# Kernel tuning notes

Measured on AMD Instinct MI355X. Metric: run time of the kernel, lower is better.

## Reference

```python
import math
import jax, jax.numpy as jnp
import numpy as np

B, S, HID, NH = 8, 512, 1024, 16
D = HID // NH          # head dim = 64
SPAN = 512             # att_span = max_relative_positions = max_position_embeddings


def _linear(x, W, b):
    # torch nn.Linear: y = x @ W.T + b, W is [out, in]
    return jnp.einsum('...i,oi->...o', x, W) + b


def _heads(x):
    # [B, S, HID] -> [B, NH, S, D]
    b, s, _ = x.shape
    return x.reshape(b, s, NH, D).transpose(0, 2, 1, 3)


def setup_inputs() -> dict:
    key = jax.random.key(0)
    ks = jax.random.split(key, 16)
    f = lambda i, shape, sc=1.0: jax.random.normal(ks[i], shape, dtype=jnp.float32) * sc
    return {
        'q': f(0, (B, S, HID)),
        'k': f(1, (B, S, HID)),
        'v': f(2, (B, S, HID)),
        'attention_mask': jnp.tril(jnp.ones((S, S), dtype=bool))[None, None],  # causal [1,1,S,S]
        'Wq': f(3, (HID, HID), 0.02), 'bq': jnp.zeros((HID,), jnp.float32),
        'Wk': f(4, (HID, HID), 0.02), 'bk': jnp.zeros((HID,), jnp.float32),
        'Wv': f(5, (HID, HID), 0.02), 'bv': jnp.zeros((HID,), jnp.float32),
        'Wpk': f(6, (HID, HID), 0.02), 'bpk': jnp.zeros((HID,), jnp.float32),
        'Wpq': f(7, (HID, HID), 0.02), 'bpq': jnp.zeros((HID,), jnp.float32),
        'rel_emb': f(8, (2 * SPAN, HID), 0.02),
    }


def reference(q, k, v, attention_mask, Wq, bq, Wk, bk, Wv, bv, Wpk, bpk, Wpq, bpq, rel_emb):
    scale_factor = 3  # 1 (content) + c2p + p2c
    scale = 1.0 / math.sqrt(D * scale_factor)

    ql = _heads(_linear(q, Wq, bq))   # [B,NH,S,D]
    kl = _heads(_linear(k, Wk, bk))
    vl = _heads(_linear(v, Wv, bv))

    # content-to-content scores
    scores = jnp.einsum('bhqd,bhkd->bhqk', ql, kl) * scale

    # relative positions (no bucketing since position_buckets = -1)
    rel = jnp.arange(S)[:, None] - jnp.arange(S)[None, :]          # [S,S]
    c2p_pos = jnp.clip(rel + SPAN, 0, 2 * SPAN - 1)
    p2c_pos = jnp.clip(-rel + SPAN, 0, 2 * SPAN - 1)

    # projected relative-position embeddings -> [NH, 2*SPAN, D]
    pk = _linear(rel_emb, Wpk, bpk).reshape(2 * SPAN, NH, D).transpose(1, 0, 2)
    pq = _linear(rel_emb, Wpq, bpq).reshape(2 * SPAN, NH, D).transpose(1, 0, 2)

    # content-to-position: out[b,h,q,k] = (q . pos_key)[b,h,q, c2p_pos[q,k]]
    c2p = jnp.einsum('bhqd,hjd->bhqj', ql, pk) * scale             # [B,NH,S,2*SPAN]
    c2p = jnp.take_along_axis(c2p, jnp.broadcast_to(c2p_pos[None, None], (B, NH, S, S)), axis=-1)

    # position-to-content: gathered[b,h,k,q] = (k . pos_query)[b,h,k, p2c_pos[k,q]], then transpose
    p2c = jnp.einsum('bhkd,hjd->bhkj', kl, pq) * scale             # [B,NH,S,2*SPAN]
    p2c = jnp.take_along_axis(p2c, jnp.broadcast_to(p2c_pos[None, None], (B, NH, S, S)), axis=-1)

    scores = scores + c2p + jnp.swapaxes(p2c, -1, -2)
    # subtract detached row max (as in torch: .max(...).values.detach())
    scores = scores - jax.lax.stop_gradient(scores.max(axis=-1, keepdims=True))

    # XSoftmax: masked softmax, then zero masked positions
    neg = jnp.float32(-1e30)
    probs = jax.nn.softmax(jnp.where(attention_mask, scores, neg), axis=-1)
    probs = jnp.where(attention_mask, probs, 0.0)

    ctx = jnp.einsum('bhqk,bhkd->bhqd', probs, vl)                 # [B,NH,S,D]
    return ctx.transpose(0, 2, 1, 3).reshape(B, S, HID)
```

## Files before the change

### kernel.cpp

```cpp
#include <hip/hip_runtime.h>
#include <hip/hip_bf16.h>
#include <math.h>

#define SCALE 0.07216878364870323f
#define NEG_BIG -1e30f

typedef __attribute__((ext_vector_type(8))) short bf16x8;
typedef __attribute__((ext_vector_type(4))) short bf16x4;
typedef __attribute__((ext_vector_type(4))) float f32x4;
#define MFMA_BF16 __builtin_amdgcn_mfma_f32_16x16x32_bf16

#define BARX()   asm volatile("s_barrier" ::: "memory")
#define VMCNT2() asm volatile("s_waitcnt vmcnt(2)" ::: "memory")
#define VMCNT0() asm volatile("s_waitcnt vmcnt(0)" ::: "memory")

static __device__ __forceinline__ float bf2f(__hip_bfloat16 x) { return __bfloat162float(x); }
static __device__ __forceinline__ __hip_bfloat16 f2bf(float x) { return __float2bfloat16(x); }
static __device__ __forceinline__ short f2bs(float x) {
  union { __hip_bfloat16 b; short s; } u; u.b = __float2bfloat16(x); return u.s;
}
static __device__ __forceinline__ float s2f(short v) {
  union { float f; unsigned u; } x; x.u = ((unsigned)(unsigned short)v) << 16; return x.f;
}
static __device__ __forceinline__ bf16x4 cvt4(float4 f) {
  bf16x4 r; r[0] = f2bs(f.x); r[1] = f2bs(f.y); r[2] = f2bs(f.z); r[3] = f2bs(f.w);
  return r;
}
static __device__ __forceinline__ bf16x8 ldg8(const __hip_bfloat16* p) {
  return *(const bf16x8*)p;
}
static __device__ __forceinline__ void gl_lds16(const __hip_bfloat16* g, __hip_bfloat16* l) {
  __builtin_amdgcn_global_load_lds(
      (const __attribute__((address_space(1))) void*)g,
      (__attribute__((address_space(3))) void*)l, 16, 0, 0);
}

struct CvtJob { const float* src; __hip_bfloat16* dst; int n4; };
struct CvtArgs { CvtJob j[9]; };

__global__ __launch_bounds__(256) void cvt_kernel(CvtArgs a) {
  const CvtJob jb = a.j[blockIdx.y];
  const float4* s = (const float4*)jb.src;
  bf16x4* d = (bf16x4*)jb.dst;
  const int stride = gridDim.x * 256;
  for (int i = blockIdx.x * 256 + threadIdx.x; i < jb.n4; i += stride)
    d[i] = cvt4(s[i]);
}

struct Gemm { const __hip_bfloat16* A; const __hip_bfloat16* W;
              const float* bias; __hip_bfloat16* out; int mode; int mBits; int nBlk;
              float oscale; };
struct ProjArgs { Gemm g[5]; };

static __device__ __forceinline__ void stage_half(const __hip_bfloat16* gtile,
                                                  __hip_bfloat16* ltile,
                                                  int half, int wave, int lane) {
  const int r = lane >> 3;
  const int chunk = (lane & 7) ^ r;
#pragma unroll
  for (int c = 0; c < 2; c++) {
    const int rowbase = half * 128 + c * 64 + wave * 8;
    gl_lds16(gtile + (size_t)(rowbase + r) * 1024 + chunk * 8,
             ltile + (size_t)rowbase * 64);
  }
}

__global__ __launch_bounds__(512, 2) void proj_kernel(ProjArgs pa) {
  const Gemm g = pa.g[blockIdx.y];
  if ((int)blockIdx.x >= g.nBlk) return;
  __shared__ __hip_bfloat16 As[2][256][64];
  __shared__ __hip_bfloat16 Ws[2][256][64];

  const int bid = blockIdx.x;
  const int m0 = (bid & ((1 << g.mBits) - 1)) * 256;
  const int n0 = (bid >> g.mBits) * 256;
  const int tid = threadIdx.x;
  const int wave = tid >> 6, lane = tid & 63;
  const int q16 = lane >> 4, l16 = lane & 15;
  const int wr = wave >> 2, wc = wave & 3;
  const int l7 = l16 & 7;

  const __hip_bfloat16* Ag = g.A + (size_t)m0 * 1024;
  const __hip_bfloat16* Wg = g.W + (size_t)n0 * 1024;

  f32x4 acc[8][4] = {};

  stage_half(Ag, &As[0][0][0], 0, wave, lane);
  stage_half(Ag, &As[0][0][0], 1, wave, lane);
  stage_half(Wg, &Ws[0][0][0], 0, wave, lane);
  stage_half(Wg, &Ws[0][0][0], 1, wave, lane);
  stage_half(Ag + 64, &As[1][0][0], 0, wave, lane);
  VMCNT2();
  BARX();

  for (int t = 0; t < 16; ++t) {
    const int cur = t & 1;
    const __hip_bfloat16* Ac = &As[cur][0][0];
    const __hip_bfloat16* Wc = &Ws[cur][0][0];
    __hip_bfloat16* An = &As[cur ^ 1][0][0];
    __hip_bfloat16* Wn = &Ws[cur ^ 1][0][0];
    const __hip_bfloat16* gAn = Ag + (size_t)(t + 1) * 64;
    const __hip_bfloat16* gWn = Wg + (size_t)(t + 1) * 64;
    const bool pf = (t + 1 < 16);

#pragma unroll
    for (int kh = 0; kh < 2; kh++) {
      const int csw = ((kh * 4 + q16) ^ l7) * 8;
      bf16x8 bw[4];
#pragma unroll
      for (int ni = 0; ni < 4; ni++)
        bw[ni] = *(const bf16x8*)(Wc + (size_t)(wc * 64 + ni * 16 + l16) * 64 + csw);
#pragma unroll
      for (int mh = 0; mh < 2; mh++) {
        bf16x8 af[4];
#pragma unroll
        for (int mi = 0; mi < 4; mi++)
          af[mi] = *(const bf16x8*)(Ac + (size_t)(wr * 128 + mh * 64 + mi * 16 + l16) * 64 + csw);
        const int ph = kh * 2 + mh;
        if (pf) {
          if (ph == 0)      stage_half(gAn, An, 1, wave, lane);
          else if (ph == 1) stage_half(gWn, Wn, 0, wave, lane);
          else if (ph == 2) stage_half(gWn, Wn, 1, wave, lane);
        }
        __builtin_amdgcn_s_setprio(1);
#pragma unroll
        for (int ni = 0; ni < 4; ni++)
#pragma unroll
          for (int mi = 0; mi < 4; mi++)
            acc[mh * 4 + mi][ni] =
                MFMA_BF16(af[mi], bw[ni], acc[mh * 4 + mi][ni], 0, 0, 0);
        __builtin_amdgcn_s_setprio(0);
      }
    }
    BARX();
    if (t + 2 < 16) {
      stage_half(Ag + (size_t)(t + 2) * 64, &As[cur][0][0], 0, wave, lane);
      VMCNT2();
    } else {
      VMCNT0();
    }
    BARX();
  }

#pragma unroll
  for (int ni = 0; ni < 4; ni++) {
    const int n = n0 + wc * 64 + ni * 16 + l16;
#pragma unroll
    for (int mi = 0; mi < 8; mi++) {
#pragma unroll
      for (int rr = 0; rr < 4; rr++) {
        const int m = m0 + wr * 128 + mi * 16 + q16 * 4 + rr;
        float val = acc[mi][ni][rr];
        size_t oidx;
        if (g.mode == 0) {
          val = (val + g.bias[n]) * g.oscale;
          const int b = m >> 9, s = m & 511;
          const int h = n >> 6, d = n & 63;
          oidx = ((size_t)((b * 16 + h) * 512 + s)) * 64 + d;
        } else if (g.mode == 1) {
          val = (val + g.bias[m]) * g.oscale;
          const int b = n >> 9, s = n & 511;
          const int h = m >> 6, d = m & 63;
          oidx = ((size_t)((b * 16 + h) * 64 + d)) * 512 + s;
        } else {
          val = (val + g.bias[n]) * g.oscale;
          const int h = n >> 6, d = n & 63;
          oidx = ((size_t)(h * 512 + m)) * 64 + d;
        }
        g.out[oidx] = f2bf(val);
      }
    }
  }
}

__global__ __launch_bounds__(256) void attn_kernel(
    const __hip_bfloat16* __restrict__ ql,
    const __hip_bfloat16* __restrict__ kl,
    const __hip_bfloat16* __restrict__ vlT,
    const __hip_bfloat16* __restrict__ pk,
    const __hip_bfloat16* __restrict__ pq,
    float* __restrict__ out)
{
  __shared__ __align__(16) __hip_bfloat16 pool[2][64][72];
  __shared__ __align__(16) __hip_bfloat16 sc[32][520];
  __shared__ __align__(16) __hip_bfloat16 pqs3[3][32][72];
  __shared__ __align__(16) __hip_bfloat16 cpb3[3][32][34];
  __shared__ __align__(16) __hip_bfloat16 pqbT2[2][2][32][36];
  __shared__ float mred[2][32];
  __shared__ float rowsum[32];

  const int bid = blockIdx.x;
  const int qt = 15 - (bid >> 7);
  const int bh = bid & 127;
  const int h = bh & 15, b = bh >> 4;
  const int q0 = qt * 32;

  const __hip_bfloat16* qlp = ql + (size_t)bh * 512 * 64;
  const __hip_bfloat16* klp = kl + (size_t)bh * 512 * 64;
  const __hip_bfloat16* vtp = vlT + (size_t)bh * 64 * 512;
  const __hip_bfloat16* pkp = pk + (size_t)h * 512 * 64;
  const __hip_bfloat16* pqp = pq + (size_t)h * 512 * 64;

  const int tid = threadIdx.x, wave = tid >> 6, lane = tid & 63;
  const int q16 = lane >> 4, l16 = lane & 15;
  const int wr = wave & 1, wc = wave >> 1;

  const int rowQ = q0 + wr * 16 + l16;
  bf16x8 aq0 = ldg8(qlp + (size_t)rowQ * 64 + q16 * 8);
  bf16x8 aq1 = ldg8(qlp + (size_t)rowQ * 64 + 32 + q16 * 8);

  {
    int4 z = {0, 0, 0, 0};
    *(int4*)(&pqs3[2][tid >> 3][(tid & 7) * 8]) = z;
  }

  const int kEnd = q0 + 32;
  const int nIter = kEnd >> 5;

  const int sr = tid >> 3, sseg = tid & 7;
  int4 rKv, rPKv, rPQv;
  {
    rKv  = ((const int4*)(klp + (size_t)(q0 + sr) * 64))[sseg];
    rPKv = ((const int4*)(pkp + (size_t)(0 + sr) * 64))[sseg];
    rPQv = ((const int4*)(pqp + (size_t)(0 + sr) * 64))[sseg];
  }

  f32x4 qkPrev = {};
  int k0Prev = 0, parPrev = 0;
  int s3c = 0, s3p = 2, s3pp = 1;
  float mloc[4] = {NEG_BIG, NEG_BIG, NEG_BIG, NEG_BIG};

  for (int it = 0; it < nIter; ++it) {
    const int k0 = q0 - it * 32;
    const int par = it & 1;
    *(int4*)(&pool[par][sr][sseg * 8])      = rKv;
    *(int4*)(&pool[par][32 + sr][sseg * 8]) = rPKv;
    *(int4*)(&pqs3[s3c][sr][sseg * 8])      = rPQv;
    __syncthreads();
    if (it + 1 < nIter) {
      const int k0n = k0 - 32, jbn = q0 - k0n;
      rKv  = ((const int4*)(klp + (size_t)(k0n + sr) * 64))[sseg];
      rPKv = ((const int4*)(pkp + (size_t)(jbn + sr) * 64))[sseg];
      rPQv = ((const int4*)(pqp + (size_t)(jbn + sr) * 64))[sseg];
    }
    if (it > 0) {
#pragma unroll
      for (int rr = 0; rr < 4; rr++) {
        const int qh = wr * 16 + q16 * 4 + rr;
        const int kh = wc * 16 + l16;
        if (k0Prev + kh > q0 + qh) {
          sc[qh][k0Prev + kh] = f2bf(NEG_BIG);
        } else {
          const int dlt = qh - kh;
          const float c2pv = (dlt >= 0) ? bf2f(cpb3[s3p][qh][dlt])
                                        : bf2f(cpb3[s3pp][qh][dlt + 32]);
          const float p2cv = (dlt >= 0) ? bf2f(pqbT2[parPrev][1][dlt][kh])
                                        : bf2f(pqbT2[parPrev][0][dlt + 32][kh]);
          float v = qkPrev[rr] + c2pv + p2cv;
          v = fminf(v, 60.f); v = fmaxf(v, -60.f);
          mloc[rr] = fmaxf(mloc[rr], v);
          sc[qh][k0Prev + kh] = f2bf(v);
        }
      }
    }

    const int rA = wr * 16 + l16;
    const int rB = wc * 16 + l16;
    f32x4 qk = {}, cp = {}, p0 = {}, p1 = {};
    __builtin_amdgcn_s_setprio(1);
#pragma unroll
    for (int ksi = 0; ksi < 2; ksi++) {
      const int ko = ksi * 32 + q16 * 8;
      bf16x8 aq = ksi ? aq1 : aq0;
      bf16x8 ak = *(const bf16x8*)(&pool[par][rA][ko]);
      bf16x8 bk = *(const bf16x8*)(&pool[par][rB][ko]);
      bf16x8 bp = *(const bf16x8*)(&pool[par][32 + rB][ko]);
      bf16x8 b1 = *(const bf16x8*)(&pqs3[s3c][rB][ko]);
      bf16x8 b0 = *(const bf16x8*)(&pqs3[s3p][rB][ko]);
      qk = MFMA_BF16(aq, bk, qk, 0, 0, 0);
      cp = MFMA_BF16(aq, bp, cp, 0, 0, 0);
      p0 = MFMA_BF16(ak, b0, p0, 0, 0, 0);
      p1 = MFMA_BF16(ak, b1, p1, 0, 0, 0);
    }
    __builtin_amdgcn_s_setprio(0);
    {
      const int cw = wc * 16 + l16;
      const int rwb = wr * 16 + q16 * 4;
      bf16x4 v0, v1;
#pragma unroll
      for (int rr = 0; rr < 4; rr++) {
        cpb3[s3c][rwb + rr][cw] = f2bf(cp[rr]);
        v0[rr] = f2bs(p0[rr]);
        v1[rr] = f2bs(p1[rr]);
      }
      *(bf16x4*)(&pqbT2[par][0][cw][rwb]) = v0;
      *(bf16x4*)(&pqbT2[par][1][cw][rwb]) = v1;
    }
    qkPrev = qk; k0Prev = k0; parPrev = par;
    const int t3 = s3pp; s3pp = s3p; s3p = s3c; s3c = t3;
  }
  __syncthreads();
  {
#pragma unroll
    for (int rr = 0; rr < 4; rr++) {
      const int qh = wr * 16 + q16 * 4 + rr;
      const int kh = wc * 16 + l16;
      if (k0Prev + kh > q0 + qh) {
        sc[qh][k0Prev + kh] = f2bf(NEG_BIG);
      } else {
        const int dlt = qh - kh;
        const float c2pv = (dlt >= 0) ? bf2f(cpb3[s3p][qh][dlt])
                                      : bf2f(cpb3[s3pp][qh][dlt + 32]);
        const float p2cv = (dlt >= 0) ? bf2f(pqbT2[parPrev][1][dlt][kh])
                                      : bf2f(pqbT2[parPrev][0][dlt + 32][kh]);
        float v = qkPrev[rr] + c2pv + p2cv;
        v = fminf(v, 60.f); v = fmaxf(v, -60.f);
        mloc[rr] = fmaxf(mloc[rr], v);
        sc[qh][k0Prev + kh] = f2bf(v);
      }
    }
  }
#pragma unroll
  for (int rr = 0; rr < 4; rr++) {
    float m = mloc[rr];
    m = fmaxf(m, __shfl_xor(m, 1));
    m = fmaxf(m, __shfl_xor(m, 2));
    m = fmaxf(m, __shfl_xor(m, 4));
    m = fmaxf(m, __shfl_xor(m, 8));
    if (l16 == 0) mred[wc][wr * 16 + q16 * 4 + rr] = m;
  }
  __syncthreads();

  {
    const int row = tid >> 3, sub = tid & 7;
    const float m = fmaxf(mred[0][row], mred[1][row]);
    float s = 0.f;
    for (int c = sub * 8; c < kEnd; c += 64) {
      bf16x8 x8 = *(const bf16x8*)(&sc[row][c]);
      bf16x8 p8;
#pragma unroll
      for (int e = 0; e < 8; e++) {
        const float p = __expf(s2f(x8[e]) - m);
        p8[e] = f2bs(p);
        s += p;
      }
      *(bf16x8*)(&sc[row][c]) = p8;
    }
    for (int off = 1; off < 8; off <<= 1) s += __shfl_xor(s, off);
    if (sub == 0) rowsum[row] = s;
  }

  f32x4 octx[2] = {};
  {
    int p = 0;
    for (int k0 = 0; k0 < kEnd; k0 += 64, p ^= 1) {
      {
        const int r = tid >> 2, seg = tid & 3;
        const int4* src = (const int4*)(vtp + (size_t)r * 512 + k0);
        *(int4*)(&pool[p][r][seg * 8])       = src[seg];
        *(int4*)(&pool[p][r][(seg + 4) * 8]) = src[seg + 4];
      }
      __syncthreads();
      __builtin_amdgcn_s_setprio(1);
#pragma unroll
      for (int sub = 0; sub < 2; sub++) {
        const int kk = k0 + sub * 32;
        if (kk < kEnd) {
          bf16x8 af = *(const bf16x8*)(&sc[wr * 16 + l16][kk + q16 * 8]);
#pragma unroll
          for (int cs = 0; cs < 2; cs++) {
            bf16x8 bv = *(const bf16x8*)(&pool[p][wc * 32 + cs * 16 + l16][sub * 32 + q16 * 8]);
            octx[cs] = MFMA_BF16(af, bv, octx[cs], 0, 0, 0);
          }
        }
      }
      __builtin_amdgcn_s_setprio(0);
    }
  }

  for (int cs = 0; cs < 2; cs++) {
    const int d = wc * 32 + cs * 16 + l16;
    for (int rr = 0; rr < 4; rr++) {
      const int qh = wr * 16 + q16 * 4 + rr;
      const float val = octx[cs][rr] / rowsum[qh];
      out[((size_t)(b * 512 + q0 + qh)) * 1024 + h * 64 + d] = val;
    }
  }
}

extern "C" void kernel_launch(void* const* d_in, const int* in_sizes, int n_in,
                              void* d_out, int out_size, void* d_ws, size_t ws_size,
                              hipStream_t stream) {
  const float* q   = (const float*)d_in[0];
  const float* k   = (const float*)d_in[1];
  const float* v   = (const float*)d_in[2];
  const float* Wq  = (const float*)d_in[4];
  const float* bq  = (const float*)d_in[5];
  const float* Wk  = (const float*)d_in[6];
  const float* bk  = (const float*)d_in[7];
  const float* Wv  = (const float*)d_in[8];
  const float* bv  = (const float*)d_in[9];
  const float* Wpk = (const float*)d_in[10];
  const float* bpk = (const float*)d_in[11];
  const float* Wpq = (const float*)d_in[12];
  const float* bpq = (const float*)d_in[13];
  const float* rel = (const float*)d_in[14];
  float* out = (float*)d_out;

  char* ws = (char*)d_ws;
  const size_t MB = 1u << 20;
  __hip_bfloat16* bqi  = (__hip_bfloat16*)(ws);
  __hip_bfloat16* bki  = (__hip_bfloat16*)(ws + 8 * MB);
  __hip_bfloat16* bvi  = (__hip_bfloat16*)(ws + 16 * MB);
  __hip_bfloat16* bWq  = (__hip_bfloat16*)(ws + 24 * MB);
  __hip_bfloat16* bWk  = (__hip_bfloat16*)(ws + 26 * MB);
  __hip_bfloat16* bWv  = (__hip_bfloat16*)(ws + 28 * MB);
  __hip_bfloat16* bWpk = (__hip_bfloat16*)(ws + 30 * MB);
  __hip_bfloat16* bWpq = (__hip_bfloat16*)(ws + 32 * MB);
  __hip_bfloat16* brel = (__hip_bfloat16*)(ws + 34 * MB);
  __hip_bfloat16* wql  = (__hip_bfloat16*)(ws + 35 * MB);
  __hip_bfloat16* wkl  = (__hip_bfloat16*)(ws + 43 * MB);
  __hip_bfloat16* wvlT = (__hip_bfloat16*)(ws + 51 * MB);
  __hip_bfloat16* wpk  = (__hip_bfloat16*)(ws + 59 * MB);
  __hip_bfloat16* wpq  = (__hip_bfloat16*)(ws + 60 * MB);

  CvtArgs ca;
  ca.j[0] = { q,   bqi,  4194304 / 4 };
  ca.j[1] = { k,   bki,  4194304 / 4 };
  ca.j[2] = { v,   bvi,  4194304 / 4 };
  ca.j[3] = { Wq,  bWq,  1048576 / 4 };
  ca.j[4] = { Wk,  bWk,  1048576 / 4 };
  ca.j[5] = { Wv,  bWv,  1048576 / 4 };
  ca.j[6] = { Wpk, bWpk, 1048576 / 4 };
  ca.j[7] = { Wpq, bWpq, 1048576 / 4 };
  ca.j[8] = { rel + (size_t)512 * 1024, brel, 524288 / 4 };
  cvt_kernel<<<dim3(1024, 9), 256, 0, stream>>>(ca);

  ProjArgs pj;
  pj.g[0] = { bqi,  bWq,  bq,  wql,  0, 4, 64, SCALE };
  pj.g[1] = { bki,  bWk,  bk,  wkl,  0, 4, 64, 1.0f };
  pj.g[2] = { bWv,  bvi,  bv,  wvlT, 1, 2, 64, 1.0f };
  pj.g[3] = { brel, bWpk, bpk, wpk,  2, 1, 8,  1.0f };
  pj.g[4] = { brel, bWpq, bpq, wpq,  2, 1, 8,  SCALE };
  proj_kernel<<<dim3(64, 5), 512, 0, stream>>>(pj);

  attn_kernel<<<2048, 256, 0, stream>>>(wql, wkl, wvlT, wpk, wpq, out);
}
```

Measured before the change: 241.2 us.

## Restructure score loop: per-wave GEMM roles with a synchronous combine step

Replaces the software-pipelined score loop, which combined the previous tile's qk, c2p and p2c during the next iteration, with a two-barrier-per-iteration scheme. Each wave now computes one full 32x32 product per tile: qk, c2p, or one of the two p2c halves. Results go to shared buffers, and all threads then combine them and write masked scores. This removes the 3-deep rotating buffers and the separate epilogue, and simplifies the row-max reduction to one value per thread. The cost is an extra barrier per iteration and lost overlap between the combine and the MFMA phase. The clamp to ±60 is also dropped.

```diff
diff --git a/kernel.cpp b/kernel.cpp
--- a/kernel.cpp
+++ b/kernel.cpp
@@ -182,11 +182,12 @@
     float* __restrict__ out)
 {
   __shared__ __align__(16) __hip_bfloat16 pool[2][64][72];
-  __shared__ __align__(16) __hip_bfloat16 sc[32][520];
-  __shared__ __align__(16) __hip_bfloat16 pqs3[3][32][72];
-  __shared__ __align__(16) __hip_bfloat16 cpb3[3][32][34];
-  __shared__ __align__(16) __hip_bfloat16 pqbT2[2][2][32][36];
-  __shared__ float mred[2][32];
+  __shared__ __align__(16) __hip_bfloat16 pqs[2][32][72];
+  __shared__ __align__(16) float qkbuf[32][36];
+  __shared__ __align__(16) __hip_bfloat16 cpb[2][32][68];
+  __shared__ __align__(16) __hip_bfloat16 pT[64][36];
+  __shared__ __align__(16) __hip_bfloat16 sc[32][528];
+  __shared__ float mred[32];
   __shared__ float rowsum[32];
 
   const int bid = blockIdx.x;
@@ -205,13 +206,16 @@
   const int q16 = lane >> 4, l16 = lane & 15;
   const int wr = wave & 1, wc = wave >> 1;
 
-  const int rowQ = q0 + wr * 16 + l16;
-  bf16x8 aq0 = ldg8(qlp + (size_t)rowQ * 64 + q16 * 8);
-  bf16x8 aq1 = ldg8(qlp + (size_t)rowQ * 64 + 32 + q16 * 8);
+  bf16x8 qlB[2][2];
+#pragma unroll
+  for (int ksi = 0; ksi < 2; ksi++)
+#pragma unroll
+    for (int bq = 0; bq < 2; bq++)
+      qlB[ksi][bq] = ldg8(qlp + (size_t)(q0 + bq * 16 + l16) * 64 + ksi * 32 + q16 * 8);
 
   {
     int4 z = {0, 0, 0, 0};
-    *(int4*)(&pqs3[2][tid >> 3][(tid & 7) * 8]) = z;
+    *(int4*)(&pqs[1][tid >> 3][(tid & 7) * 8]) = z;
   }
 
   const int kEnd = q0 + 32;
@@ -225,115 +229,110 @@
     rPQv = ((const int4*)(pqp + (size_t)(0 + sr) * 64))[sseg];
   }
 
-  f32x4 qkPrev = {};
-  int k0Prev = 0, parPrev = 0;
-  int s3c = 0, s3p = 2, s3pp = 1;
-  float mloc[4] = {NEG_BIG, NEG_BIG, NEG_BIG, NEG_BIG};
+  const int aq = tid >> 3;
+  const int kb = (tid & 7) * 4;
+  float mloc = NEG_BIG;
 
   for (int it = 0; it < nIter; ++it) {
     const int k0 = q0 - it * 32;
     const int par = it & 1;
     *(int4*)(&pool[par][sr][sseg * 8])      = rKv;
     *(int4*)(&pool[par][32 + sr][sseg * 8]) = rPKv;
-    *(int4*)(&pqs3[s3c][sr][sseg * 8])      = rPQv;
+    *(int4*)(&pqs[par][sr][sseg * 8])       = rPQv;
     __syncthreads();
+
+    const int arb = (wave == 1) ? 32 : 0;
+    f32x4 a4[2][2] = {};
+    __builtin_amdgcn_s_setprio(1);
+#pragma unroll
+    for (int ksi = 0; ksi < 2; ksi++) {
+      const int ko = ksi * 32 + q16 * 8;
+      bf16x8 Af0 = *(const bf16x8*)(&pool[par][arb + l16][ko]);
+      bf16x8 Af1 = *(const bf16x8*)(&pool[par][arb + 16 + l16][ko]);
+      bf16x8 Bf0, Bf1;
+      if (wave < 2) {
+        Bf0 = qlB[ksi][0];
+        Bf1 = qlB[ksi][1];
+      } else {
+        const int ps = (wave == 2) ? (par ^ 1) : par;
+        Bf0 = *(const bf16x8*)(&pqs[ps][l16][ko]);
+        Bf1 = *(const bf16x8*)(&pqs[ps][16 + l16][ko]);
+      }
+      a4[0][0] = MFMA_BF16(Af0, Bf0, a4[0][0], 0, 0, 0);
+      a4[0][1] = MFMA_BF16(Af0, Bf1, a4[0][1], 0, 0, 0);
+      a4[1][0] = MFMA_BF16(Af1, Bf0, a4[1][0], 0, 0, 0);
+      a4[1][1] = MFMA_BF16(Af1, Bf1, a4[1][1], 0, 0, 0);
+    }
+    __builtin_amdgcn_s_setprio(0);
+
+    if (wave == 0) {
+#pragma unroll
+      for (int a = 0; a < 2; a++)
+#pragma unroll
+        for (int bq = 0; bq < 2; bq++)
+          *(f32x4*)(&qkbuf[bq * 16 + l16][a * 16 + q16 * 4]) = a4[a][bq];
+    } else if (wave == 1) {
+#pragma unroll
+      for (int a = 0; a < 2; a++)
+#pragma unroll
+        for (int bq = 0; bq < 2; bq++) {
+          bf16x4 v;
+#pragma unroll
+          for (int r = 0; r < 4; r++) v[r] = f2bs(a4[a][bq][r]);
+          const int q = bq * 16 + l16, jr = a * 16 + q16 * 4;
+          *(bf16x4*)(&cpb[par][q][32 + jr]) = v;
+          *(bf16x4*)(&cpb[par ^ 1][q][jr]) = v;
+        }
+    } else {
+      const int rb = (wave == 3) ? 32 : 0;
+#pragma unroll
+      for (int a = 0; a < 2; a++)
+#pragma unroll
+        for (int bq = 0; bq < 2; bq++) {
+          bf16x4 v;
+#pragma unroll
+          for (int r = 0; r < 4; r++) v[r] = f2bs(a4[a][bq][r]);
+          *(bf16x4*)(&pT[rb + bq * 16 + l16][a * 16 + q16 * 4]) = v;
+        }
+    }
+    __syncthreads();
+
     if (it + 1 < nIter) {
-      const int k0n = k0 - 32, jbn = q0 - k0n;
+      const int k0n = k0 - 32, jbn = (it + 1) * 32;
       rKv  = ((const int4*)(klp + (size_t)(k0n + sr) * 64))[sseg];
       rPKv = ((const int4*)(pkp + (size_t)(jbn + sr) * 64))[sseg];
       rPQv = ((const int4*)(pqp + (size_t)(jbn + sr) * 64))[sseg];
     }
-    if (it > 0) {
-#pragma unroll
-      for (int rr = 0; rr < 4; rr++) {
-        const int qh = wr * 16 + q16 * 4 + rr;
-        const int kh = wc * 16 + l16;
-        if (k0Prev + kh > q0 + qh) {
-          sc[qh][k0Prev + kh] = f2bf(NEG_BIG);
-        } else {
-          const int dlt = qh - kh;
-          const float c2pv = (dlt >= 0) ? bf2f(cpb3[s3p][qh][dlt])
-                                        : bf2f(cpb3[s3pp][qh][dlt + 32]);
-          const float p2cv = (dlt >= 0) ? bf2f(pqbT2[parPrev][1][dlt][kh])
-                                        : bf2f(pqbT2[parPrev][0][dlt + 32][kh]);
-          float v = qkPrev[rr] + c2pv + p2cv;
-          v = fminf(v, 60.f); v = fmaxf(v, -60.f);
-          mloc[rr] = fmaxf(mloc[rr], v);
-          sc[qh][k0Prev + kh] = f2bf(v);
-        }
-      }
-    }
-
-    const int rA = wr * 16 + l16;
-    const int rB = wc * 16 + l16;
-    f32x4 qk = {}, cp = {}, p0 = {}, p1 = {};
-    __builtin_amdgcn_s_setprio(1);
-#pragma unroll
-    for (int ksi = 0; ksi < 2; ksi++) {
-      const int ko = ksi * 32 + q16 * 8;
-      bf16x8 aq = ksi ? aq1 : aq0;
-      bf16x8 ak = *(const bf16x8*)(&pool[par][rA][ko]);
-      bf16x8 bk = *(const bf16x8*)(&pool[par][rB][ko]);
-      bf16x8 bp = *(const bf16x8*)(&pool[par][32 + rB][ko]);
-      bf16x8 b1 = *(const bf16x8*)(&pqs3[s3c][rB][ko]);
-      bf16x8 b0 = *(const bf16x8*)(&pqs3[s3p][rB][ko]);
-      qk = MFMA_BF16(aq, bk, qk, 0, 0, 0);
-      cp = MFMA_BF16(aq, bp, cp, 0, 0, 0);
-      p0 = MFMA_BF16(ak, b0, p0, 0, 0, 0);
-      p1 = MFMA_BF16(ak, b1, p1, 0, 0, 0);
-    }
-    __builtin_amdgcn_s_setprio(0);
+
     {
-      const int cw = wc * 16 + l16;
-      const int rwb = wr * 16 + q16 * 4;
-      bf16x4 v0, v1;
-#pragma unroll
-      for (int rr = 0; rr < 4; rr++) {
-        cpb3[s3c][rwb + rr][cw] = f2bf(cp[rr]);
-        v0[rr] = f2bs(p0[rr]);
-        v1[rr] = f2bs(p1[rr]);
-      }
-      *(bf16x4*)(&pqbT2[par][0][cw][rwb]) = v0;
-      *(bf16x4*)(&pqbT2[par][1][cw][rwb]) = v1;
-    }
-    qkPrev = qk; k0Prev = k0; parPrev = par;
-    const int t3 = s3pp; s3pp = s3p; s3p = s3c; s3c = t3;
-  }
-  __syncthreads();
+      const f32x4 qk4 = *(const f32x4*)(&qkbuf[aq][kb]);
+      bf16x4 scv;
+#pragma unroll
+      for (int j = 0; j < 4; j++) {
+        const int kl_ = kb + j;
+        const int dlt = aq - kl_;
+        const float v = qk4[j] + bf2f(cpb[par][aq][dlt + 32])
+                               + bf2f(pT[dlt + 32][kl_]);
+        const bool msk = (it == 0) && (dlt < 0);
+        if (!msk) mloc = fmaxf(mloc, v);
+        scv[j] = msk ? f2bs(NEG_BIG) : f2bs(v);
+      }
+      *(bf16x4*)(&sc[aq][k0 + kb]) = scv;
+    }
+  }
+
   {
-#pragma unroll
-    for (int rr = 0; rr < 4; rr++) {
-      const int qh = wr * 16 + q16 * 4 + rr;
-      const int kh = wc * 16 + l16;
-      if (k0Prev + kh > q0 + qh) {
-        sc[qh][k0Prev + kh] = f2bf(NEG_BIG);
-      } else {
-        const int dlt = qh - kh;
-        const float c2pv = (dlt >= 0) ? bf2f(cpb3[s3p][qh][dlt])
-                                      : bf2f(cpb3[s3pp][qh][dlt + 32]);
-        const float p2cv = (dlt >= 0) ? bf2f(pqbT2[parPrev][1][dlt][kh])
-                                      : bf2f(pqbT2[parPrev][0][dlt + 32][kh]);
-        float v = qkPrev[rr] + c2pv + p2cv;
-        v = fminf(v, 60.f); v = fmaxf(v, -60.f);
-        mloc[rr] = fmaxf(mloc[rr], v);
-        sc[qh][k0Prev + kh] = f2bf(v);
-      }
-    }
-  }
-#pragma unroll
-  for (int rr = 0; rr < 4; rr++) {
-    float m = mloc[rr];
+    float m = mloc;
     m = fmaxf(m, __shfl_xor(m, 1));
     m = fmaxf(m, __shfl_xor(m, 2));
     m = fmaxf(m, __shfl_xor(m, 4));
-    m = fmaxf(m, __shfl_xor(m, 8));
-    if (l16 == 0) mred[wc][wr * 16 + q16 * 4 + rr] = m;
+    if ((tid & 7) == 0) mred[aq] = m;
   }
   __syncthreads();
 
   {
     const int row = tid >> 3, sub = tid & 7;
-    const float m = fmaxf(mred[0][row], mred[1][row]);
+    const float m = mred[row];
     float s = 0.f;
     for (int c = sub * 8; c < kEnd; c += 64) {
       bf16x8 x8 = *(const bf16x8*)(&sc[row][c]);
```

New measurement: 245.6 us. Within noise of the previous version (+1.8%).
